# Performance work log

Hardware: AMD Instinct MI355X
Metric: run time of the kernel (lower is better)

The kernel has to match this reference:

```python
import jax, jax.numpy as jnp
import numpy as np

B, LV, D = 8, 4096, 256   # batch, temporal length, channels
N = 2048                   # total ROIs across the batch
P = 32                     # output_size (number of output bins)
G = int(np.ceil(LV / P))   # static max adaptive sampling grid (sampling_ratio=-1)


def setup_inputs() -> dict:
    key = jax.random.key(0)
    k1, k2, k3 = jax.random.split(key, 3)
    feat = jax.random.normal(k1, (B, LV, D), dtype=jnp.float32)
    # boxes: (start, end) along the lv axis, sorted so start <= end, in [0, LV)
    boxes = jnp.sort(
        jax.random.uniform(k2, (N, 2), dtype=jnp.float32, minval=0.0, maxval=float(LV)),
        axis=1,
    )
    batch_idx = jax.random.randint(k3, (N,), 0, B, dtype=jnp.int32)
    return {"feat": feat, "boxes": boxes, "batch_idx": batch_idx}


def _roi_align_1d(feat, boxes, batch_idx):
    # Faithful 1D specialization of torchvision roi_align with boxes
    # (0, y1, 1, y2), output_size=(P, 1), aligned=True, spatial_scale=1,
    # sampling_ratio=-1. The width axis contributes a single sample at x=0
    # with weight 1, so only the y (lv) axis math remains.
    feat_flat = feat.reshape(B * LV, D)
    y1, y2 = boxes[:, 0], boxes[:, 1]
    roi_h = y2 - y1                       # aligned=True: no max(., 1) clamp
    start = y1 - 0.5                      # aligned offset
    bin_h = roi_h / P                     # [N]
    grid_h = jnp.ceil(bin_h).astype(jnp.int32)          # adaptive samples per bin
    count = jnp.maximum(grid_h, 1).astype(feat.dtype)   # avg denominator
    sub = bin_h / jnp.maximum(grid_h, 1)                # spacing inside a bin [N]
    # bin start positions: [N, P]
    bin_off = start[:, None] + jnp.arange(P, dtype=feat.dtype)[None, :] * bin_h[:, None]
    base = batch_idx.astype(jnp.int32) * LV             # [N] row offset into feat_flat

    def bilinear(y):  # y: [N, P] -> [N, P, D]
        valid = (y >= -1.0) & (y <= float(LV))
        yc = jnp.maximum(y, 0.0)
        y_lo = jnp.floor(yc).astype(jnp.int32)
        hi_case = y_lo >= LV - 1
        y_lo = jnp.where(hi_case, LV - 1, y_lo)
        y_hi = jnp.where(hi_case, LV - 1, y_lo + 1)
        yc = jnp.where(hi_case, y_lo.astype(y.dtype), yc)
        ly = yc - y_lo.astype(y.dtype)
        v = (1.0 - ly)[..., None] * feat_flat[base[:, None] + y_lo] \
            + ly[..., None] * feat_flat[base[:, None] + y_hi]
        return jnp.where(valid[..., None], v, 0.0)

    def step(acc, g):
        y = bin_off + (g.astype(feat.dtype) + 0.5) * sub[:, None]   # [N, P]
        m = (g < grid_h)[:, None, None]                              # sample active?
        return acc + jnp.where(m, bilinear(y), 0.0), None

    acc0 = jnp.zeros((N, P, D), dtype=feat.dtype)
    acc, _ = jax.lax.scan(step, acc0, jnp.arange(G, dtype=jnp.int32))
    return acc / count[:, None, None]   # [N, P, D] (torch output after transpose(1,2))


def reference(feat, boxes, batch_idx):
    return _roi_align_1d(feat, boxes, batch_idx)
```

## Files before the change

### kernel.cpp

```cpp
#include <hip/hip_runtime.h>

#define B_     8
#define LV_    4096
#define D_     256
#define N_     2048
#define P_     32
#define WROWS_ 64
#define NWIN_  (B_ * (LV_ / WROWS_))
#define NBINS_ (N_ * P_)
#define CAP_   256
#define CPB_   32
#define SEGS_  (CAP_ / CPB_)
#define NGW_   (NWIN_ * SEGS_)
#define NOVF_  64

typedef float v4f __attribute__((ext_vector_type(4)));

__device__ __forceinline__ float lane_bcast_f(float v, int l) {
    return __int_as_float(__builtin_amdgcn_readlane(__float_as_int(v), l));
}

__device__ __forceinline__ int bin_r_first(const float* __restrict__ boxes, int n, int p) {
    const float y1 = boxes[2 * n], y2 = boxes[2 * n + 1];
    const float bin_h = (y2 - y1) * (1.0f / (float)P_);
    const int gh = (int)ceilf(bin_h);
    if (gh < 1) return 0;
    const float sub  = bin_h / (float)gh;
    const float boff = (y1 - 0.5f) + (float)p * bin_h;
    const float a    = fmaf(0.5f, sub, boff);
    int r = (int)floorf(a);
    if (r < 0) r = 0;
    if (r > LV_ - 1) r = LV_ - 1;
    return r;
}

__global__ __launch_bounds__(256) void scatter_bins_kernel(
    const float* __restrict__ boxes, const int* __restrict__ batch_idx,
    int* __restrict__ wsp)
{
    int* cnt    = wsp;
    int* ovfc   = wsp + NWIN_;
    int* bucket = wsp + 1024;
    int* ovf    = bucket + NWIN_ * CAP_;
    const int idx = blockIdx.x * 256 + threadIdx.x;
    const int n = idx >> 5, p = idx & 31;
    const int key = (batch_idx[n] << 6) | (bin_r_first(boxes, n, p) >> 6);
    const int slot = atomicAdd(&cnt[key], 1);
    if (slot < CAP_) bucket[key * CAP_ + slot] = idx;
    else             ovf[atomicAdd(ovfc, 1)] = idx;
}

__device__ __forceinline__ void process_bin(
    const float* __restrict__ feat, const float* __restrict__ boxes,
    const int* __restrict__ batch_idx, float* __restrict__ out,
    const v4f* tile, int wb, int wlo, int idx, int lane)
{
    const int n = idx >> 5, p = idx & 31;
    const int bi = __builtin_amdgcn_readfirstlane(batch_idx[n]);

    const float y1 = boxes[2 * n], y2 = boxes[2 * n + 1];
    const float bin_h = (y2 - y1) * (1.0f / (float)P_);
    const int gh = (int)ceilf(bin_h);

    const v4f* prow = (const v4f*)feat + (long)bi * (LV_ * (D_ / 4));
    v4f acc0 = {0.f,0.f,0.f,0.f}, acc1 = {0.f,0.f,0.f,0.f};

    if (gh >= 1) {
        const float cntf = (float)gh, sub = bin_h / cntf, inv_sub = 1.0f / sub;
        const float halfsub = 0.5f * sub;
        const float boff = (y1 - 0.5f) + (float)p * bin_h;
        const float a = fmaf(0.5f, sub, boff), ylast = fmaf(cntf - 0.5f, sub, boff);

        int r_first = (int)floorf(a);
        if (r_first < 0) r_first = 0; if (r_first > LV_-1) r_first = LV_-1;
        int r_last = (int)floorf(ylast) + 1;
        if (r_last > LV_-1) r_last = LV_-1; if (r_last < r_first) r_last = r_first;
        const int r0 = __builtin_amdgcn_readfirstlane(r_first);
        const int rl = __builtin_amdgcn_readfirstlane(r_last);
        const float lanef = (float)lane;

        for (int gbase = r0; gbase <= rl; gbase += 64) {
            int kmax = rl - gbase; if (kmax > 63) kmax = 63;

            const int   r  = gbase + lane;
            const float d0 = ((float)gbase + lanef) - a;
            const float dm = d0 - 1.0f, dp = d0 + 1.0f;
            const float nm = fminf(fmaxf(ceilf(dm * inv_sub), 0.0f), cntf);
            const float n0 = fminf(fmaxf(ceilf(d0 * inv_sub), 0.0f), cntf);
            const float np = fminf(fmaxf(ceilf(dp * inv_sub), 0.0f), cntf);
            float Pm = fmaf(nm, dm, -halfsub * fmaf(nm, nm, -nm));
            float P0 = fmaf(n0, d0, -halfsub * fmaf(n0, n0, -n0));
            float Pp = fmaf(np, dp, -halfsub * fmaf(np, np, -np));
            if (r == 0)       Pm = P0;
            if (r == LV_ - 1) Pp = P0 + cntf;
            const float Wl = (Pm + Pp) - 2.0f * P0;

            const int t = kmax + 1;
            int lo, hi;
            if (tile && bi == wb) {
                lo = wlo - gbase;          lo = lo < 0 ? 0 : (lo > t ? t : lo);
                hi = wlo + WROWS_ - gbase; hi = hi < lo ? lo : (hi > t ? t : hi);
            } else { lo = t; hi = t; }

#define GSEG(KS, KE) do {                                                        \
    int k = (KS);                                                                \
    const v4f* pS = prow + (long)(gbase + k) * (D_ / 4);                         \
    for (; k + 4 <= (KE); k += 4) {                                              \
        v4f v0 = pS[lane], v1 = pS[lane+64], v2 = pS[lane+128], v3 = pS[lane+192];\
        acc0 += v0 * lane_bcast_f(Wl, k);   acc1 += v1 * lane_bcast_f(Wl, k+1);  \
        acc0 += v2 * lane_bcast_f(Wl, k+2); acc1 += v3 * lane_bcast_f(Wl, k+3);  \
        pS += 4 * (D_ / 4); }                                                    \
    for (; k < (KE); ++k) { v4f v = pS[lane]; acc0 += v * lane_bcast_f(Wl, k); pS += (D_ / 4); } \
} while (0)

            GSEG(0, lo);
            {
                int k = lo;
                const v4f* tp = tile + (gbase + lo - wlo) * 64 + lane;
                for (; k + 4 <= hi; k += 4) {
                    v4f t0 = tp[0], t1 = tp[64], t2 = tp[128], t3 = tp[192];
                    acc0 += t0 * lane_bcast_f(Wl, k);   acc1 += t1 * lane_bcast_f(Wl, k+1);
                    acc0 += t2 * lane_bcast_f(Wl, k+2); acc1 += t3 * lane_bcast_f(Wl, k+3);
                    tp += 256;
                }
                for (; k < hi; ++k) { acc0 += tp[0] * lane_bcast_f(Wl, k); tp += 64; }
            }
            GSEG(hi, t);
#undef GSEG
        }
    }

    const float inv_c = 1.0f / (float)(gh > 1 ? gh : 1);
    v4f res = (acc0 + acc1) * inv_c;
    v4f* op = (v4f*)out + ((long)n * P_ + p) * (D_ / 4) + lane;
    __builtin_nontemporal_store(res, op);
}

__global__ __launch_bounds__(512) void roi_win_kernel(
    const float* __restrict__ feat, const float* __restrict__ boxes,
    const int* __restrict__ batch_idx, const int* __restrict__ wsp,
    float* __restrict__ out)
{
    __shared__ v4f tile[WROWS_ * 64];
    const int* cnt    = wsp;
    const int* ovfc   = wsp + NWIN_;
    const int* bucket = wsp + 1024;
    const int* ovf    = bucket + NWIN_ * CAP_;

    const int tid  = threadIdx.x;
    const int lane = tid & 63;
    const int wv   = tid >> 6;
    const int bid  = blockIdx.x;

    if (bid >= NGW_) {
        const int no = ovfc[0];
        for (int j = (bid - NGW_) * 8 + wv; j < no; j += NOVF_ * 8) {
            const int idx = __builtin_amdgcn_readfirstlane(ovf[j]);
            process_bin(feat, boxes, batch_idx, out, nullptr, 0, 0, idx, lane);
        }
        return;
    }

    const int blk = (bid & 7) * (NGW_ / 8) + (bid >> 3);
    const int w   = blk >> 3;
    const int seg = blk & (SEGS_ - 1);

    const int total = min(cnt[w], CAP_);
    const int start = seg * CPB_;
    if (start >= total) return;
    const int nb = min(CPB_, total - start);

    const int wb  = w >> 6;
    const int wlo = (w & 63) << 6;

    {
        const int r0 = wv * 8;
        const float* srow = feat + ((long)wb * LV_ + wlo + r0) * D_ + lane * 4;
        v4f* lrow = tile + r0 * 64;
#if __has_builtin(__builtin_amdgcn_global_load_lds)
        #pragma unroll
        for (int j = 0; j < 8; ++j) {
            __builtin_amdgcn_global_load_lds(
                (const __attribute__((address_space(1))) void*)(srow + j * D_),
                (__attribute__((address_space(3))) void*)(lrow + j * 64),
                16, 0, 0);
        }
#else
        const v4f* src = (const v4f*)feat + ((long)wb * LV_ + wlo + r0) * (D_ / 4) + lane;
        v4f t0 = src[0],   t1 = src[64],  t2 = src[128], t3 = src[192];
        v4f t4 = src[256], t5 = src[320], t6 = src[384], t7 = src[448];
        v4f* dst = lrow + lane;
        dst[0]   = t0; dst[64]  = t1; dst[128] = t2; dst[192] = t3;
        dst[256] = t4; dst[320] = t5; dst[384] = t6; dst[448] = t7;
#endif
    }
    __syncthreads();

    for (int i = wv; i < nb; i += 8) {
        const int idx = __builtin_amdgcn_readfirstlane(bucket[w * CAP_ + start + i]);
        process_bin(feat, boxes, batch_idx, out, tile, wb, wlo, idx, lane);
    }
}

__global__ __launch_bounds__(256) void build_order_kernel(
    const int* __restrict__ batch_idx, int* __restrict__ order)
{
    __shared__ int cnt[B_], cur[B_];
    const int tid = threadIdx.x;
    if (tid < B_) cnt[tid] = 0;
    __syncthreads();
    for (int n = tid; n < N_; n += 256) atomicAdd(&cnt[batch_idx[n]], 1);
    __syncthreads();
    if (tid == 0) { int s = 0; for (int b = 0; b < B_; ++b) { cur[b] = s; s += cnt[b]; } }
    __syncthreads();
    for (int n = tid; n < N_; n += 256)
        order[atomicAdd(&cur[batch_idx[n]], 1)] = n;
}

__global__ __launch_bounds__(256) void roi_rows_kernel(
    const float* __restrict__ feat, const float* __restrict__ boxes,
    const int* __restrict__ batch_idx, const int* __restrict__ order,
    float* __restrict__ out)
{
    const int nwg = (N_ * P_) / 4;
    const int cpx = nwg >> 3;
    const int bid = blockIdx.x;
    const int swz = (bid & 7) * cpx + (bid >> 3);
    const int slot = (swz << 2) + (threadIdx.x >> 6);
    const int n    = __builtin_amdgcn_readfirstlane(order[slot >> 5]);
    const int p    = slot & (P_ - 1);
    const int lane = threadIdx.x & 63;
    process_bin(feat, boxes, batch_idx, out, nullptr, 0, 0, (n << 5) | p, lane);
}

extern "C" void kernel_launch(void* const* d_in, const int* in_sizes, int n_in,
                              void* d_out, int out_size, void* d_ws, size_t ws_size,
                              hipStream_t stream) {
    const float* feat      = (const float*)d_in[0];
    const float* boxes     = (const float*)d_in[1];
    const int*   batch_idx = (const int*)d_in[2];
    float*       out       = (float*)d_out;

    const size_t need = (size_t)(1024 + NWIN_ * CAP_ + NBINS_) * sizeof(int);
    if (ws_size >= need) {
        int* wsp = (int*)d_ws;
        hipMemsetAsync(wsp, 0, (NWIN_ + 1) * sizeof(int), stream);
        scatter_bins_kernel<<<NBINS_ / 256, 256, 0, stream>>>(boxes, batch_idx, wsp);
        roi_win_kernel<<<NGW_ + NOVF_, 512, 0, stream>>>(feat, boxes, batch_idx, wsp, out);
    } else {
        int* order = (int*)d_ws;
        build_order_kernel<<<1, 256, 0, stream>>>(batch_idx, order);
        roi_rows_kernel<<<(N_ * P_) / 4, 256, 0, stream>>>(feat, boxes, batch_idx, order, out);
    }
}
```

Baseline: 222.2 us.

## Replace atomic window bucketing with per-batch ROI scan inside window blocks

```diff
diff --git a/kernel.cpp b/kernel.cpp
--- a/kernel.cpp
+++ b/kernel.cpp
@@ -6,13 +6,9 @@
 #define N_     2048
 #define P_     32
 #define WROWS_ 64
+#define SEGS_  4
 #define NWIN_  (B_ * (LV_ / WROWS_))
-#define NBINS_ (N_ * P_)
-#define CAP_   256
-#define CPB_   32
-#define SEGS_  (CAP_ / CPB_)
-#define NGW_   (NWIN_ * SEGS_)
-#define NOVF_  64
+#define NBLK_  (NWIN_ * SEGS_)
 
 typedef float v4f __attribute__((ext_vector_type(4)));
 
@@ -34,20 +30,23 @@
     return r;
 }
 
-__global__ __launch_bounds__(256) void scatter_bins_kernel(
-    const float* __restrict__ boxes, const int* __restrict__ batch_idx,
-    int* __restrict__ wsp)
-{
-    int* cnt    = wsp;
-    int* ovfc   = wsp + NWIN_;
-    int* bucket = wsp + 1024;
-    int* ovf    = bucket + NWIN_ * CAP_;
-    const int idx = blockIdx.x * 256 + threadIdx.x;
-    const int n = idx >> 5, p = idx & 31;
-    const int key = (batch_idx[n] << 6) | (bin_r_first(boxes, n, p) >> 6);
-    const int slot = atomicAdd(&cnt[key], 1);
-    if (slot < CAP_) bucket[key * CAP_ + slot] = idx;
-    else             ovf[atomicAdd(ovfc, 1)] = idx;
+__global__ __launch_bounds__(256) void build_order_kernel(
+    const int* __restrict__ batch_idx, int* __restrict__ order, int* __restrict__ offs)
+{
+    __shared__ int cnt[B_], cur[B_];
+    const int tid = threadIdx.x;
+    if (tid < B_) cnt[tid] = 0;
+    __syncthreads();
+    for (int n = tid; n < N_; n += 256) atomicAdd(&cnt[batch_idx[n]], 1);
+    __syncthreads();
+    if (tid == 0) {
+        int s = 0;
+        for (int b = 0; b < B_; ++b) { cur[b] = s; offs[b] = s; s += cnt[b]; }
+        offs[B_] = s;
+    }
+    __syncthreads();
+    for (int n = tid; n < N_; n += 256)
+        order[atomicAdd(&cur[batch_idx[n]], 1)] = n;
 }
 
 __device__ __forceinline__ void process_bin(
@@ -138,40 +137,37 @@
 
 __global__ __launch_bounds__(512) void roi_win_kernel(
     const float* __restrict__ feat, const float* __restrict__ boxes,
-    const int* __restrict__ batch_idx, const int* __restrict__ wsp,
-    float* __restrict__ out)
+    const int* __restrict__ batch_idx, const int* __restrict__ order,
+    const int* __restrict__ offs, float* __restrict__ out)
 {
     __shared__ v4f tile[WROWS_ * 64];
-    const int* cnt    = wsp;
-    const int* ovfc   = wsp + NWIN_;
-    const int* bucket = wsp + 1024;
-    const int* ovf    = bucket + NWIN_ * CAP_;
+    __shared__ int flag;
 
     const int tid  = threadIdx.x;
     const int lane = tid & 63;
     const int wv   = tid >> 6;
     const int bid  = blockIdx.x;
 
-    if (bid >= NGW_) {
-        const int no = ovfc[0];
-        for (int j = (bid - NGW_) * 8 + wv; j < no; j += NOVF_ * 8) {
-            const int idx = __builtin_amdgcn_readfirstlane(ovf[j]);
-            process_bin(feat, boxes, batch_idx, out, nullptr, 0, 0, idx, lane);
-        }
-        return;
-    }
-
-    const int blk = (bid & 7) * (NGW_ / 8) + (bid >> 3);
-    const int w   = blk >> 3;
+    const int blk = (bid & 7) * (NBLK_ / 8) + (bid >> 3);
+    const int w   = blk >> 2;
     const int seg = blk & (SEGS_ - 1);
-
-    const int total = min(cnt[w], CAP_);
-    const int start = seg * CPB_;
-    if (start >= total) return;
-    const int nb = min(CPB_, total - start);
-
     const int wb  = w >> 6;
-    const int wlo = (w & 63) << 6;
+    const int wt  = w & 63;
+    const int wlo = wt << 6;
+
+    const int off_b = offs[wb];
+    const int cnt_b = offs[wb + 1] - off_b;
+
+    if (tid == 0) flag = 0;
+    __syncthreads();
+    for (int jj = tid; jj < cnt_b; jj += 512) {
+        const int n = order[off_b + jj];
+        const int rlo = bin_r_first(boxes, n, 0);
+        const int rhi = bin_r_first(boxes, n, P_ - 1);
+        if (rlo < wlo + WROWS_ && rhi >= wlo) { flag = 1; break; }
+    }
+    __syncthreads();
+    if (!flag) return;
 
     {
         const int r0 = wv * 8;
@@ -196,41 +192,51 @@
     }
     __syncthreads();
 
-    for (int i = wv; i < nb; i += 8) {
-        const int idx = __builtin_amdgcn_readfirstlane(bucket[w * CAP_ + start + i]);
-        process_bin(feat, boxes, batch_idx, out, tile, wb, wlo, idx, lane);
-    }
-}
-
-__global__ __launch_bounds__(256) void build_order_kernel(
-    const int* __restrict__ batch_idx, int* __restrict__ order)
-{
-    __shared__ int cnt[B_], cur[B_];
-    const int tid = threadIdx.x;
-    if (tid < B_) cnt[tid] = 0;
-    __syncthreads();
-    for (int n = tid; n < N_; n += 256) atomicAdd(&cnt[batch_idx[n]], 1);
-    __syncthreads();
-    if (tid == 0) { int s = 0; for (int b = 0; b < B_; ++b) { cur[b] = s; s += cnt[b]; } }
-    __syncthreads();
-    for (int n = tid; n < N_; n += 256)
-        order[atomicAdd(&cur[batch_idx[n]], 1)] = n;
-}
-
-__global__ __launch_bounds__(256) void roi_rows_kernel(
+    for (int j = seg + SEGS_ * wv; j < cnt_b; j += SEGS_ * 8) {
+        const int n = __builtin_amdgcn_readfirstlane(order[off_b + j]);
+
+        const float y1 = boxes[2 * n], y2 = boxes[2 * n + 1];
+        const float bin_h = (y2 - y1) * (1.0f / (float)P_);
+        const int gh = (int)ceilf(bin_h);
+
+        int pl_c, width;
+        if (bin_h > 1e-6f) {
+            const float sub   = bin_h / (float)(gh < 1 ? 1 : gh);
+            const float A0    = (y1 - 0.5f) + 0.5f * sub;
+            const float invbh = 1.0f / bin_h;
+            const float plf = (wt == 0)  ? 0.0f  : ((float)wlo - A0) * invbh - 1.0f;
+            const float phf = (wt == 63) ? 32.0f : ((float)(wlo + WROWS_) - A0) * invbh + 1.0f;
+            int pl = (int)floorf(fminf(fmaxf(plf, 0.0f), 32.0f));
+            int ph = (int)ceilf(fminf(fmaxf(phf, 0.0f), 32.0f));
+            if (ph < pl) ph = pl;
+            pl_c = pl; width = ph - pl;
+        } else {
+            pl_c = 0; width = 32;
+        }
+        if (width == 0) continue;
+
+        bool in = false;
+        if (lane < width) {
+            const int p = pl_c + lane;
+            in = ((bin_r_first(boxes, n, p) >> 6) == wt);
+        }
+        const unsigned long long m = __ballot(in);
+        if (!m) continue;
+        const int pl   = pl_c + __builtin_ctzll(m);
+        const int pcnt = __builtin_popcountll(m);
+
+        for (int pp = pl; pp < pl + pcnt; ++pp)
+            process_bin(feat, boxes, batch_idx, out, tile, wb, wlo, (n << 5) | pp, lane);
+    }
+}
+
+__global__ __launch_bounds__(256) void roi_plain_kernel(
     const float* __restrict__ feat, const float* __restrict__ boxes,
-    const int* __restrict__ batch_idx, const int* __restrict__ order,
-    float* __restrict__ out)
-{
-    const int nwg = (N_ * P_) / 4;
-    const int cpx = nwg >> 3;
-    const int bid = blockIdx.x;
-    const int swz = (bid & 7) * cpx + (bid >> 3);
-    const int slot = (swz << 2) + (threadIdx.x >> 6);
-    const int n    = __builtin_amdgcn_readfirstlane(order[slot >> 5]);
-    const int p    = slot & (P_ - 1);
+    const int* __restrict__ batch_idx, float* __restrict__ out)
+{
+    const int slot = blockIdx.x * 4 + (threadIdx.x >> 6);
     const int lane = threadIdx.x & 63;
-    process_bin(feat, boxes, batch_idx, out, nullptr, 0, 0, (n << 5) | p, lane);
+    process_bin(feat, boxes, batch_idx, out, nullptr, 0, 0, slot, lane);
 }
 
 extern "C" void kernel_launch(void* const* d_in, const int* in_sizes, int n_in,
@@ -241,15 +247,12 @@
     const int*   batch_idx = (const int*)d_in[2];
     float*       out       = (float*)d_out;
 
-    const size_t need = (size_t)(1024 + NWIN_ * CAP_ + NBINS_) * sizeof(int);
-    if (ws_size >= need) {
-        int* wsp = (int*)d_ws;
-        hipMemsetAsync(wsp, 0, (NWIN_ + 1) * sizeof(int), stream);
-        scatter_bins_kernel<<<NBINS_ / 256, 256, 0, stream>>>(boxes, batch_idx, wsp);
-        roi_win_kernel<<<NGW_ + NOVF_, 512, 0, stream>>>(feat, boxes, batch_idx, wsp, out);
+    if (ws_size >= (size_t)(N_ + B_ + 1) * sizeof(int)) {
+        int* order = (int*)d_ws;
+        int* offs  = order + N_;
+        build_order_kernel<<<1, 256, 0, stream>>>(batch_idx, order, offs);
+        roi_win_kernel<<<NBLK_, 512, 0, stream>>>(feat, boxes, batch_idx, order, offs, out);
     } else {
-        int* order = (int*)d_ws;
-        build_order_kernel<<<1, 256, 0, stream>>>(batch_idx, order);
-        roi_rows_kernel<<<(N_ * P_) / 4, 256, 0, stream>>>(feat, boxes, batch_idx, order, out);
-    }
-}
+        roi_plain_kernel<<<(N_ * P_) / 4, 256, 0, stream>>>(feat, boxes, batch_idx, out);
+    }
+}
```

Result: faster. 203.6 us (-8.3%).
